# Optimization experiments

Measured on AMD Instinct MI355X. Metric: run time of the kernel, lower is better.

Reference implementation:

```python
import jax, jax.numpy as jnp
import numpy as np

B, C_IN, H, W = 4, 256, 48, 48
HEADS, HD = 8, 64
N = H * W
SCALE = 1.0 / (HD ** 0.5)


def setup_inputs() -> dict:
    key = jax.random.key(0)
    ks = jax.random.split(key, 5)
    x = jax.random.normal(ks[0], (B, C_IN, H, W), dtype=jnp.float32)
    # 1x1 conv weights, squeezed: [heads, head_channels, in_channels]
    Wq = jax.random.normal(ks[1], (HEADS, HD, C_IN), dtype=jnp.float32) * (C_IN ** -0.5)
    Wk = jax.random.normal(ks[2], (HEADS, HD, C_IN), dtype=jnp.float32) * (C_IN ** -0.5)
    Wv = jax.random.normal(ks[3], (HEADS, HD, C_IN), dtype=jnp.float32) * (C_IN ** -0.5)
    # output 1x1 conv: [in_channels, heads*head_channels]
    Wo = jax.random.normal(ks[4], (C_IN, HEADS * HD), dtype=jnp.float32) * ((HEADS * HD) ** -0.5)
    return {"x": x, "Wq": Wq, "Wk": Wk, "Wv": Wv, "Wo": Wo}


def reference(x, Wq, Wk, Wv, Wo):
    b, c, h, w = x.shape
    n = h * w
    xf = x.reshape(b, c, n)  # [B, C, N]
    # per-head 1x1 convs == batched projections -> [heads, B, N, HD]
    q = jnp.einsum('hdc,bcn->hbnd', Wq, xf)
    k = jnp.einsum('hdc,bcn->hbnd', Wk, xf)
    v = jnp.einsum('hdc,bcn->hbnd', Wv, xf)
    scores = jnp.einsum('hbnd,hbmd->hbnm', q, k) * SCALE  # [heads, B, N, N]
    probs = jax.nn.softmax(scores, axis=-1)
    ws = jnp.einsum('hbnm,hbmd->hbnd', probs, v)  # [heads, B, N, HD]
    # faithful replication of torch: transpose(1,2) then reshape(B, heads*HD, H, W)
    ws = jnp.transpose(ws, (0, 2, 1, 3))  # [heads, N, B, HD]
    ws = ws.reshape(b, HEADS * HD, h, w)
    out = jnp.einsum('oc,bchw->bohw', Wo, ws)  # output 1x1 conv
    return out
```

## Files before the change

### kernel.cpp

```cpp
#include <hip/hip_runtime.h>

#define B_     4
#define CIN    256
#define NTOK   2304
#define HEADS  8
#define HD     64
#define SCALE  0.125f
#define LOG2E  1.44269504088896f
#define QSCALE (SCALE * LOG2E)
#define PBIAS  4.0f
#define QKV_ELEMS (HEADS * B_ * NTOK * HD)
#define HBSTRIDE 147456
#define WSZ    131072

typedef _Float16 f16;
typedef _Float16 __attribute__((ext_vector_type(8))) h8v;
typedef _Float16 __attribute__((ext_vector_type(4))) h4v;
typedef ushort   __attribute__((ext_vector_type(8))) us8;
typedef float    __attribute__((ext_vector_type(16))) f16v;

__device__ inline uint pk2(float a, float b) {
    auto v = __builtin_amdgcn_cvt_pkrtz(a, b);
    return __builtin_bit_cast(uint, v);
}
#define EXP2(x) __builtin_amdgcn_exp2f(x)

#define GLOAD_LDS(g, l) __builtin_amdgcn_global_load_lds( \
    (const __attribute__((address_space(1))) unsigned int*)(g), \
    (__attribute__((address_space(3))) unsigned int*)(l), 16, 0, 0)

__global__ __launch_bounds__(256) void prep(
    const float* __restrict__ x,
    const float* __restrict__ Wq, const float* __restrict__ Wk,
    const float* __restrict__ Wv, const float* __restrict__ Wo,
    f16* __restrict__ wc, f16* __restrict__ woc, f16* __restrict__ xt)
{
    __shared__ float T[64][65];
    const int bid = blockIdx.x;
    const int tid = threadIdx.x;

    if (bid < 512) {
        int e4 = (bid * 256 + tid) * 4;
        const float* src; f16* dst; float mult = 1.0f; int off;
        if (e4 < WSZ)          { src = Wq; off = e4;           dst = wc;           mult = QSCALE; }
        else if (e4 < 2 * WSZ) { src = Wk; off = e4 - WSZ;     dst = wc + WSZ; }
        else if (e4 < 3 * WSZ) { src = Wv; off = e4 - 2 * WSZ; dst = wc + 2 * WSZ; }
        else                   { src = Wo; off = e4 - 3 * WSZ; dst = woc; }
        float4 r = *(const float4*)(src + off);
        h4v hv;
        hv.x = (f16)(r.x * mult); hv.y = (f16)(r.y * mult);
        hv.z = (f16)(r.z * mult); hv.w = (f16)(r.w * mult);
        *(h4v*)(dst + off) = hv;
        return;
    }

    const int r  = bid - 512;
    const int n0 = (r % 36) * 64;
    const int c0 = ((r / 36) % 4) * 64;
    const int b  = r / 144;
    const float* sb = x + ((size_t)b * CIN + c0) * NTOK;
    #pragma unroll
    for (int i = 0; i < 16; ++i) {
        int idx = tid + 256 * i;
        int rr = idx >> 6, ll = idx & 63;
        T[ll][rr] = sb[(size_t)rr * NTOK + n0 + ll];
    }
    __syncthreads();
    const size_t ob = ((size_t)b * NTOK + n0) * CIN + c0;
    #pragma unroll
    for (int i = 0; i < 4; ++i) {
        int idx = tid + 256 * i;
        int row = idx >> 4, c4 = (idx & 15) * 4;
        h4v v;
        v.x = (f16)T[row][c4 + 0]; v.y = (f16)T[row][c4 + 1];
        v.z = (f16)T[row][c4 + 2]; v.w = (f16)T[row][c4 + 3];
        *(h4v*)(xt + ob + (size_t)row * CIN + c4) = v;
    }
}

__global__ __launch_bounds__(128) void proj_mfma(
    const f16* __restrict__ wc, const f16* __restrict__ xt,
    f16* __restrict__ qh, f16* __restrict__ kh, f16* __restrict__ vth)
{
    const int ntile = blockIdx.x;
    const int hp    = blockIdx.y;
    const int b     = blockIdx.z;
    const int p     = hp >> 3, h = hp & 7;
    const int hb    = h * 4 + b;
    const f16* Wp = wc + ((size_t)p * 8 + h) * (HD * CIN);

    __shared__ __align__(16) f16 Ws[2][64][64], Xs[2][64][64];

    const int tid = threadIdx.x;
    const int w = tid >> 6, lane = tid & 63;
    const int lm = lane & 31, lh = lane >> 5;
    const int n_loc  = w * 32 + lm;
    const int n_glob = ntile * 64 + n_loc;

    const f16* xb = xt + ((size_t)b * NTOK + ntile * 64) * CIN;

    auto stage = [&](int buf, int c0) {
        const f16* src = (w == 0) ? Wp : xb;
        f16* dst = (w == 0) ? &Ws[buf][0][0] : &Xs[buf][0][0];
        #pragma unroll
        for (int i = 0; i < 8; ++i) {
            int g = i * 64 + lane; int row = g >> 3; int c = (g & 7) ^ (row & 7);
            GLOAD_LDS(src + (size_t)row * CIN + c0 + c * 8, dst + i * 512);
        }
    };

    f16v o0, o1;
    #pragma unroll
    for (int i = 0; i < 16; ++i) { o0[i] = 0.f; o1[i] = 0.f; }

    stage(0, 0);
    for (int c0 = 0; c0 < CIN; c0 += 64) {
        const int cur = (c0 >> 6) & 1;
        __syncthreads();
        if (c0 + 64 < CIN) stage(cur ^ 1, c0 + 64);
        #pragma unroll
        for (int s = 0; s < 4; ++s) {
            const int pp = ((2 * s + lh) ^ (lm & 7)) * 8;
            h8v a0 = *(const h8v*)&Ws[cur][lm][pp];
            h8v a1 = *(const h8v*)&Ws[cur][lm + 32][pp];
            h8v bh = *(const h8v*)&Xs[cur][n_loc][pp];
            o0 = __builtin_amdgcn_mfma_f32_32x32x16_f16(a0, bh, o0, 0, 0, 0);
            o1 = __builtin_amdgcn_mfma_f32_32x32x16_f16(a1, bh, o1, 0, 0, 0);
        }
    }

    const size_t hboff = (size_t)hb * HBSTRIDE;
    if (p < 2) {
        f16* oh = ((p == 0) ? qh : kh) + hboff + (size_t)n_glob * 64;
        #pragma unroll
        for (int t = 0; t < 2; ++t) {
            const f16v& oc = t ? o1 : o0;
            #pragma unroll
            for (int g = 0; g < 4; ++g) {
                int d0 = 8 * g + 4 * lh + 32 * t;
                h4v hv;
                hv.x = (f16)oc[4 * g + 0]; hv.y = (f16)oc[4 * g + 1];
                hv.z = (f16)oc[4 * g + 2]; hv.w = (f16)oc[4 * g + 3];
                *(h4v*)(oh + d0) = hv;
            }
        }
    } else {
        f16* oh = vth + hboff;
        #pragma unroll
        for (int t = 0; t < 2; ++t) {
            const f16v& oc = t ? o1 : o0;
            #pragma unroll
            for (int r = 0; r < 16; ++r) {
                int d = (r & 3) + 8 * (r >> 2) + 4 * lh + 32 * t;
                oh[(size_t)d * NTOK + n_glob] = (f16)oc[r];
            }
        }
    }
}

__global__ __launch_bounds__(128, 2) void attn_mfma(
    const f16* __restrict__ qh, const f16* __restrict__ kh,
    const f16* __restrict__ vth, f16* __restrict__ wsth)
{
    const int bid   = blockIdx.x;
    const int xcd   = bid & 7;
    const int slot  = bid >> 3;
    const int hb    = xcd * 4 + (slot / 18);
    const int rtile = slot % 18;
    const int h_    = hb >> 2, b = hb & 3;
    const int tid   = threadIdx.x;
    const int w     = tid >> 6;
    const int lane  = tid & 63;
    const int lm    = lane & 31;
    const int lh    = lane >> 5;

    __shared__ __align__(16) f16 SMEM[2][2][64][64];

    const size_t hboff = (size_t)hb * HBSTRIDE;
    const int mA = rtile * 128 + w * 64 + lm;
    const int mB = mA + 32;

    h8v QfA[4], QfB[4];
    #pragma unroll
    for (int s = 0; s < 4; ++s) {
        QfA[s] = *(const h8v*)(qh + hboff + (size_t)mA * 64 + (2 * s + lh) * 8);
        QfB[s] = *(const h8v*)(qh + hboff + (size_t)mB * 64 + (2 * s + lh) * 8);
    }

    f16v oA0, oA1, oB0, oB1;
    #pragma unroll
    for (int i = 0; i < 16; ++i) { oA0[i] = 0.f; oA1[i] = 0.f; oB0[i] = 0.f; oB1[i] = 0.f; }
    float lsumA = 0.f, lsumB = 0.f;

    const f16* gb = (w == 0) ? kh + hboff : vth + hboff;

    auto stage = [&](int buf, int kt) {
        f16* dst = &SMEM[buf][w][0][0];
        #pragma unroll
        for (int i = 0; i < 8; ++i) {
            int g   = i * 64 + lane;
            int row = g >> 3;
            int c   = (g & 7) ^ (row & 7);
            const f16* src = (w == 0)
                ? gb + kt * 4096 + row * 64 + c * 8
                : gb + (size_t)row * 2304 + kt * 64 + c * 8;
            GLOAD_LDS(src, dst + i * 512);
        }
    };

    stage(0, 0);
    __syncthreads();

    for (int kt = 0; kt < 36; ++kt) {
        const int cur = kt & 1;
        if (kt + 1 < 36) stage(cur ^ 1, kt + 1);

        f16v sA0, sA1, sB0, sB1;
        #pragma unroll
        for (int i = 0; i < 16; ++i) {
            sA0[i] = -PBIAS; sA1[i] = -PBIAS; sB0[i] = -PBIAS; sB1[i] = -PBIAS;
        }

        __builtin_amdgcn_s_setprio(1);
        #pragma unroll
        for (int s = 0; s < 4; ++s) {
            const int p = ((2 * s + lh) ^ (lm & 7)) * 8;
            h8v k0 = *(const h8v*)&SMEM[cur][0][lm][p];
            h8v k1 = *(const h8v*)&SMEM[cur][0][lm + 32][p];
            sA0 = __builtin_amdgcn_mfma_f32_32x32x16_f16(k0, QfA[s], sA0, 0, 0, 0);
            sA1 = __builtin_amdgcn_mfma_f32_32x32x16_f16(k1, QfA[s], sA1, 0, 0, 0);
            sB0 = __builtin_amdgcn_mfma_f32_32x32x16_f16(k0, QfB[s], sB0, 0, 0, 0);
            sB1 = __builtin_amdgcn_mfma_f32_32x32x16_f16(k1, QfB[s], sB1, 0, 0, 0);
        }
        __builtin_amdgcn_s_setprio(0);

        float rsA = 0.f, rsB = 0.f;
        #pragma unroll
        for (int i = 0; i < 16; ++i) { sA0[i] = EXP2(sA0[i]); rsA += sA0[i]; }
        #pragma unroll
        for (int i = 0; i < 16; ++i) { sA1[i] = EXP2(sA1[i]); rsA += sA1[i]; }
        #pragma unroll
        for (int i = 0; i < 16; ++i) { sB0[i] = EXP2(sB0[i]); rsB += sB0[i]; }
        #pragma unroll
        for (int i = 0; i < 16; ++i) { sB1[i] = EXP2(sB1[i]); rsB += sB1[i]; }
        lsumA += rsA; lsumB += rsB;

        uint PpkA[2][8], PpkB[2][8];
        #pragma unroll
        for (int pr = 0; pr < 8; ++pr) {
            PpkA[0][pr] = pk2(sA0[2 * pr], sA0[2 * pr + 1]);
            PpkA[1][pr] = pk2(sA1[2 * pr], sA1[2 * pr + 1]);
            PpkB[0][pr] = pk2(sB0[2 * pr], sB0[2 * pr + 1]);
            PpkB[1][pr] = pk2(sB1[2 * pr], sB1[2 * pr + 1]);
        }

        h8v pfA[4], pfB[4];
        #pragma unroll
        for (int s = 0; s < 4; ++s) {
            const int jt = s >> 1, q = 4 * (s & 1);
            auto a02 = __builtin_amdgcn_permlane32_swap(
                PpkA[jt][q + 0], PpkA[jt][q + 2], false, false);
            auto a13 = __builtin_amdgcn_permlane32_swap(
                PpkA[jt][q + 1], PpkA[jt][q + 3], false, false);
            uint4 ua = { a02[0], a13[0], a02[1], a13[1] };
            pfA[s] = __builtin_bit_cast(h8v, ua);
            auto b02 = __builtin_amdgcn_permlane32_swap(
                PpkB[jt][q + 0], PpkB[jt][q + 2], false, false);
            auto b13 = __builtin_amdgcn_permlane32_swap(
                PpkB[jt][q + 1], PpkB[jt][q + 3], false, false);
            uint4 ub = { b02[0], b13[0], b02[1], b13[1] };
            pfB[s] = __builtin_bit_cast(h8v, ub);
        }

        __builtin_amdgcn_s_setprio(1);
        #pragma unroll
        for (int s = 0; s < 4; ++s) {
            const int p = ((2 * s + lh) ^ (lm & 7)) * 8;
            h8v v0 = *(const h8v*)&SMEM[cur][1][lm][p];
            h8v v1 = *(const h8v*)&SMEM[cur][1][lm + 32][p];
            oA0 = __builtin_amdgcn_mfma_f32_32x32x16_f16(v0, pfA[s], oA0, 0, 0, 0);
            oA1 = __builtin_amdgcn_mfma_f32_32x32x16_f16(v1, pfA[s], oA1, 0, 0, 0);
            oB0 = __builtin_amdgcn_mfma_f32_32x32x16_f16(v0, pfB[s], oB0, 0, 0, 0);
            oB1 = __builtin_amdgcn_mfma_f32_32x32x16_f16(v1, pfB[s], oB1, 0, 0, 0);
        }
        __builtin_amdgcn_s_setprio(0);

        __syncthreads();
    }

    lsumA += __shfl_xor(lsumA, 32);
    lsumB += __shfl_xor(lsumB, 32);
    float invA = 1.0f / lsumA, invB = 1.0f / lsumB;

    f16* wrA = wsth + ((size_t)h_ * NTOK + mA) * 256 + b * 64;
    f16* wrB = wsth + ((size_t)h_ * NTOK + mB) * 256 + b * 64;
    #pragma unroll
    for (int g = 0; g < 4; ++g) {
        h4v r0, r1;
        r0.x = (f16)(oA0[4 * g + 0] * invA); r0.y = (f16)(oA0[4 * g + 1] * invA);
        r0.z = (f16)(oA0[4 * g + 2] * invA); r0.w = (f16)(oA0[4 * g + 3] * invA);
        *(h4v*)(wrA + 8 * g + 4 * lh) = r0;
        r1.x = (f16)(oA1[4 * g + 0] * invA); r1.y = (f16)(oA1[4 * g + 1] * invA);
        r1.z = (f16)(oA1[4 * g + 2] * invA); r1.w = (f16)(oA1[4 * g + 3] * invA);
        *(h4v*)(wrA + 32 + 8 * g + 4 * lh) = r1;
    }
    #pragma unroll
    for (int g = 0; g < 4; ++g) {
        h4v r0, r1;
        r0.x = (f16)(oB0[4 * g + 0] * invB); r0.y = (f16)(oB0[4 * g + 1] * invB);
        r0.z = (f16)(oB0[4 * g + 2] * invB); r0.w = (f16)(oB0[4 * g + 3] * invB);
        *(h4v*)(wrB + 8 * g + 4 * lh) = r0;
        r1.x = (f16)(oB1[4 * g + 0] * invB); r1.y = (f16)(oB1[4 * g + 1] * invB);
        r1.z = (f16)(oB1[4 * g + 2] * invB); r1.w = (f16)(oB1[4 * g + 3] * invB);
        *(h4v*)(wrB + 32 + 8 * g + 4 * lh) = r1;
    }
}

__global__ __launch_bounds__(128) void outconv_mfma(
    const f16* __restrict__ woc, const f16* __restrict__ ws,
    float* __restrict__ out)
{
    const int ntile = blockIdx.x;
    const int otile = blockIdx.y;
    const int b     = blockIdx.z;

    __shared__ __align__(16) f16 Wos[2][64][64];
    __shared__ __align__(16) f16 Xs[2][64][72];

    const int tid = threadIdx.x;
    const int w = tid >> 6, lane = tid & 63;
    const int lm = lane & 31, lh = lane >> 5;
    const int n_loc  = w * 32 + lm;
    const int n_glob = ntile * 64 + n_loc;
    const int pr = tid >> 2;
    const int qn = tid & 3;

    const f16* Wb = woc + (size_t)(otile * 64) * 512;
    const f16* wsb = ws + (size_t)b * 512 * NTOK + ntile * 64 + qn * 16;

    auto stageW = [&](int buf, int c0) {
        #pragma unroll
        for (int j = 0; j < 4; ++j) {
            int i = w * 4 + j;
            int g = i * 64 + lane; int row = g >> 3; int c = (g & 7) ^ (row & 7);
            GLOAD_LDS(Wb + (size_t)row * 512 + c0 + c * 8,
                      &Wos[buf][0][0] + i * 512);
        }
    };

    uint4 x0, x1, x2, x3;
    auto loadB = [&](int c0) {
        const f16* r0 = wsb + (size_t)(c0 + 2 * pr) * NTOK;
        const f16* r1 = r0 + NTOK;
        x0 = *(const uint4*)(r0);
        x1 = *(const uint4*)(r0 + 8);
        x2 = *(const uint4*)(r1);
        x3 = *(const uint4*)(r1 + 8);
    };
    auto storeB = [&](int buf) {
        us8 a0 = __builtin_bit_cast(us8, x0), a1 = __builtin_bit_cast(us8, x1);
        us8 b0 = __builtin_bit_cast(us8, x2), b1 = __builtin_bit_cast(us8, x3);
        #pragma unroll
        for (int j = 0; j < 8; ++j) {
            *(uint*)&Xs[buf][qn * 16 + j][2 * pr]     = (uint)a0[j] | ((uint)b0[j] << 16);
            *(uint*)&Xs[buf][qn * 16 + 8 + j][2 * pr] = (uint)a1[j] | ((uint)b1[j] << 16);
        }
    };

    f16v o0, o1;
    #pragma unroll
    for (int i = 0; i < 16; ++i) { o0[i] = 0.f; o1[i] = 0.f; }

    stageW(0, 0);
    loadB(0);
    storeB(0);
    for (int c0 = 0; c0 < 512; c0 += 64) {
        const int cur = (c0 >> 6) & 1;
        __syncthreads();
        if (c0 + 64 < 512) { stageW(cur ^ 1, c0 + 64); loadB(c0 + 64); }
        #pragma unroll
        for (int s = 0; s < 4; ++s) {
            const int pp = ((2 * s + lh) ^ (lm & 7)) * 8;
            const int co = (2 * s + lh) * 8;
            h8v a0 = *(const h8v*)&Wos[cur][lm][pp];
            h8v a1 = *(const h8v*)&Wos[cur][lm + 32][pp];
            h8v bh = *(const h8v*)&Xs[cur][n_loc][co];
            o0 = __builtin_amdgcn_mfma_f32_32x32x16_f16(a0, bh, o0, 0, 0, 0);
            o1 = __builtin_amdgcn_mfma_f32_32x32x16_f16(a1, bh, o1, 0, 0, 0);
        }
        if (c0 + 64 < 512) storeB(cur ^ 1);
    }

    #pragma unroll
    for (int t = 0; t < 2; ++t) {
        const f16v& oc = t ? o1 : o0;
        #pragma unroll
        for (int r = 0; r < 16; ++r) {
            int orow = otile * 64 + (r & 3) + 8 * (r >> 2) + 4 * lh + 32 * t;
            out[((size_t)b * CIN + orow) * NTOK + n_glob] = oc[r];
        }
    }
}

extern "C" void kernel_launch(void* const* d_in, const int* in_sizes, int n_in,
                              void* d_out, int out_size, void* d_ws, size_t ws_size,
                              hipStream_t stream)
{
    const float* x  = (const float*)d_in[0];
    const float* Wq = (const float*)d_in[1];
    const float* Wk = (const float*)d_in[2];
    const float* Wv = (const float*)d_in[3];
    const float* Wo = (const float*)d_in[4];
    float* out = (float*)d_out;

    f16* qh   = (f16*)d_ws;
    f16* kh   = qh   + QKV_ELEMS;
    f16* vth  = kh   + QKV_ELEMS;
    f16* wsth = vth  + QKV_ELEMS;
    f16* xt   = wsth;
    f16* wc   = wsth + QKV_ELEMS;
    f16* woc  = wc   + 3 * WSZ;

    prep<<<dim3(1088), 256, 0, stream>>>(x, Wq, Wk, Wv, Wo, wc, woc, xt);
    proj_mfma<<<dim3(36, 24, 4), 128, 0, stream>>>(wc, xt, qh, kh, vth);
    attn_mfma<<<dim3(576), 128, 0, stream>>>(qh, kh, vth, wsth);
    outconv_mfma<<<dim3(36, 4, 4), 128, 0, stream>>>(woc, wsth, out);
}
```

Before: 178.9 us.

## Split attention key loop across wave pairs with LDS reduction of partial outputs

```diff
diff --git a/kernel.cpp b/kernel.cpp
--- a/kernel.cpp
+++ b/kernel.cpp
@@ -158,7 +158,7 @@
     }
 }
 
-__global__ __launch_bounds__(128, 2) void attn_mfma(
+__global__ __launch_bounds__(256, 2) void attn_mfma(
     const f16* __restrict__ qh, const f16* __restrict__ kh,
     const f16* __restrict__ vth, f16* __restrict__ wsth)
 {
@@ -166,18 +166,21 @@
     const int xcd   = bid & 7;
     const int slot  = bid >> 3;
     const int hb    = xcd * 4 + (slot / 18);
-    const int rtile = slot % 18;
+    const int rpair = slot % 18;
     const int h_    = hb >> 2, b = hb & 3;
     const int tid   = threadIdx.x;
     const int w     = tid >> 6;
     const int lane  = tid & 63;
     const int lm    = lane & 31;
     const int lh    = lane >> 5;
+    const int qg    = w >> 1;
+    const int ks    = w & 1;
 
     __shared__ __align__(16) f16 SMEM[2][2][64][64];
+    __shared__ float LRED[256];
 
     const size_t hboff = (size_t)hb * HBSTRIDE;
-    const int mA = rtile * 128 + w * 64 + lm;
+    const int mA = rpair * 128 + qg * 64 + lm;
     const int mB = mA + 32;
 
     h8v QfA[4], QfB[4];
@@ -192,29 +195,29 @@
     for (int i = 0; i < 16; ++i) { oA0[i] = 0.f; oA1[i] = 0.f; oB0[i] = 0.f; oB1[i] = 0.f; }
     float lsumA = 0.f, lsumB = 0.f;
 
-    const f16* gb = (w == 0) ? kh + hboff : vth + hboff;
-
-    auto stage = [&](int buf, int kt) {
-        f16* dst = &SMEM[buf][w][0][0];
+    const int  sv  = w >> 1;
+    const int  stp = w & 1;
+    const f16* gb  = (sv == 0) ? kh + hboff : vth + hboff;
+
+    auto stage = [&](int st) {
+        const int kts = 2 * st + stp;
+        f16* dst = &SMEM[sv][stp][0][0];
         #pragma unroll
         for (int i = 0; i < 8; ++i) {
             int g   = i * 64 + lane;
             int row = g >> 3;
             int c   = (g & 7) ^ (row & 7);
-            const f16* src = (w == 0)
-                ? gb + kt * 4096 + row * 64 + c * 8
-                : gb + (size_t)row * 2304 + kt * 64 + c * 8;
+            const f16* src = (sv == 0)
+                ? gb + kts * 4096 + row * 64 + c * 8
+                : gb + (size_t)row * 2304 + kts * 64 + c * 8;
             GLOAD_LDS(src, dst + i * 512);
         }
     };
 
-    stage(0, 0);
+    stage(0);
     __syncthreads();
 
-    for (int kt = 0; kt < 36; ++kt) {
-        const int cur = kt & 1;
-        if (kt + 1 < 36) stage(cur ^ 1, kt + 1);
-
+    for (int st = 0; st < 18; ++st) {
         f16v sA0, sA1, sB0, sB1;
         #pragma unroll
         for (int i = 0; i < 16; ++i) {
@@ -225,8 +228,8 @@
         #pragma unroll
         for (int s = 0; s < 4; ++s) {
             const int p = ((2 * s + lh) ^ (lm & 7)) * 8;
-            h8v k0 = *(const h8v*)&SMEM[cur][0][lm][p];
-            h8v k1 = *(const h8v*)&SMEM[cur][0][lm + 32][p];
+            h8v k0 = *(const h8v*)&SMEM[0][ks][lm][p];
+            h8v k1 = *(const h8v*)&SMEM[0][ks][lm + 32][p];
             sA0 = __builtin_amdgcn_mfma_f32_32x32x16_f16(k0, QfA[s], sA0, 0, 0, 0);
             sA1 = __builtin_amdgcn_mfma_f32_32x32x16_f16(k1, QfA[s], sA1, 0, 0, 0);
             sB0 = __builtin_amdgcn_mfma_f32_32x32x16_f16(k0, QfB[s], sB0, 0, 0, 0);
@@ -234,16 +237,41 @@
         }
         __builtin_amdgcn_s_setprio(0);
 
-        float rsA = 0.f, rsB = 0.f;
-        #pragma unroll
-        for (int i = 0; i < 16; ++i) { sA0[i] = EXP2(sA0[i]); rsA += sA0[i]; }
-        #pragma unroll
-        for (int i = 0; i < 16; ++i) { sA1[i] = EXP2(sA1[i]); rsA += sA1[i]; }
-        #pragma unroll
-        for (int i = 0; i < 16; ++i) { sB0[i] = EXP2(sB0[i]); rsB += sB0[i]; }
-        #pragma unroll
-        for (int i = 0; i < 16; ++i) { sB1[i] = EXP2(sB1[i]); rsB += sB1[i]; }
-        lsumA += rsA; lsumB += rsB;
+        __syncthreads();
+        if (st + 1 < 18 && sv == 0) stage(st + 1);
+
+        float pa0 = 0.f, pa1 = 0.f, pa2 = 0.f, pa3 = 0.f;
+        float pb0 = 0.f, pb1 = 0.f, pb2 = 0.f, pb3 = 0.f;
+        #pragma unroll
+        for (int i = 0; i < 16; i += 4) {
+            sA0[i+0] = EXP2(sA0[i+0]); pa0 += sA0[i+0];
+            sA0[i+1] = EXP2(sA0[i+1]); pa1 += sA0[i+1];
+            sA0[i+2] = EXP2(sA0[i+2]); pa2 += sA0[i+2];
+            sA0[i+3] = EXP2(sA0[i+3]); pa3 += sA0[i+3];
+        }
+        #pragma unroll
+        for (int i = 0; i < 16; i += 4) {
+            sA1[i+0] = EXP2(sA1[i+0]); pa0 += sA1[i+0];
+            sA1[i+1] = EXP2(sA1[i+1]); pa1 += sA1[i+1];
+            sA1[i+2] = EXP2(sA1[i+2]); pa2 += sA1[i+2];
+            sA1[i+3] = EXP2(sA1[i+3]); pa3 += sA1[i+3];
+        }
+        #pragma unroll
+        for (int i = 0; i < 16; i += 4) {
+            sB0[i+0] = EXP2(sB0[i+0]); pb0 += sB0[i+0];
+            sB0[i+1] = EXP2(sB0[i+1]); pb1 += sB0[i+1];
+            sB0[i+2] = EXP2(sB0[i+2]); pb2 += sB0[i+2];
+            sB0[i+3] = EXP2(sB0[i+3]); pb3 += sB0[i+3];
+        }
+        #pragma unroll
+        for (int i = 0; i < 16; i += 4) {
+            sB1[i+0] = EXP2(sB1[i+0]); pb0 += sB1[i+0];
+            sB1[i+1] = EXP2(sB1[i+1]); pb1 += sB1[i+1];
+            sB1[i+2] = EXP2(sB1[i+2]); pb2 += sB1[i+2];
+            sB1[i+3] = EXP2(sB1[i+3]); pb3 += sB1[i+3];
+        }
+        lsumA += (pa0 + pa1) + (pa2 + pa3);
+        lsumB += (pb0 + pb1) + (pb2 + pb3);
 
         uint PpkA[2][8], PpkB[2][8];
         #pragma unroll
@@ -276,8 +304,8 @@
         #pragma unroll
         for (int s = 0; s < 4; ++s) {
             const int p = ((2 * s + lh) ^ (lm & 7)) * 8;
-            h8v v0 = *(const h8v*)&SMEM[cur][1][lm][p];
-            h8v v1 = *(const h8v*)&SMEM[cur][1][lm + 32][p];
+            h8v v0 = *(const h8v*)&SMEM[1][ks][lm][p];
+            h8v v1 = *(const h8v*)&SMEM[1][ks][lm + 32][p];
             oA0 = __builtin_amdgcn_mfma_f32_32x32x16_f16(v0, pfA[s], oA0, 0, 0, 0);
             oA1 = __builtin_amdgcn_mfma_f32_32x32x16_f16(v1, pfA[s], oA1, 0, 0, 0);
             oB0 = __builtin_amdgcn_mfma_f32_32x32x16_f16(v0, pfB[s], oB0, 0, 0, 0);
@@ -286,33 +314,58 @@
         __builtin_amdgcn_s_setprio(0);
 
         __syncthreads();
-    }
-
-    lsumA += __shfl_xor(lsumA, 32);
-    lsumB += __shfl_xor(lsumB, 32);
-    float invA = 1.0f / lsumA, invB = 1.0f / lsumB;
-
-    f16* wrA = wsth + ((size_t)h_ * NTOK + mA) * 256 + b * 64;
-    f16* wrB = wsth + ((size_t)h_ * NTOK + mB) * 256 + b * 64;
-    #pragma unroll
-    for (int g = 0; g < 4; ++g) {
-        h4v r0, r1;
-        r0.x = (f16)(oA0[4 * g + 0] * invA); r0.y = (f16)(oA0[4 * g + 1] * invA);
-        r0.z = (f16)(oA0[4 * g + 2] * invA); r0.w = (f16)(oA0[4 * g + 3] * invA);
-        *(h4v*)(wrA + 8 * g + 4 * lh) = r0;
-        r1.x = (f16)(oA1[4 * g + 0] * invA); r1.y = (f16)(oA1[4 * g + 1] * invA);
-        r1.z = (f16)(oA1[4 * g + 2] * invA); r1.w = (f16)(oA1[4 * g + 3] * invA);
-        *(h4v*)(wrA + 32 + 8 * g + 4 * lh) = r1;
-    }
-    #pragma unroll
-    for (int g = 0; g < 4; ++g) {
-        h4v r0, r1;
-        r0.x = (f16)(oB0[4 * g + 0] * invB); r0.y = (f16)(oB0[4 * g + 1] * invB);
-        r0.z = (f16)(oB0[4 * g + 2] * invB); r0.w = (f16)(oB0[4 * g + 3] * invB);
-        *(h4v*)(wrB + 8 * g + 4 * lh) = r0;
-        r1.x = (f16)(oB1[4 * g + 0] * invB); r1.y = (f16)(oB1[4 * g + 1] * invB);
-        r1.z = (f16)(oB1[4 * g + 2] * invB); r1.w = (f16)(oB1[4 * g + 3] * invB);
-        *(h4v*)(wrB + 32 + 8 * g + 4 * lh) = r1;
+        if (st + 1 < 18 && sv == 1) stage(st + 1);
+    }
+
+    float* red = (float*)&SMEM[0][0][0][0];
+    if (ks == 1) {
+        float* dA = red + (size_t)(qg * 128 + lane) * 32;
+        float* dB = red + (size_t)(qg * 128 + 64 + lane) * 32;
+        #pragma unroll
+        for (int i = 0; i < 16; ++i) {
+            dA[i] = oA0[i]; dA[16 + i] = oA1[i];
+            dB[i] = oB0[i]; dB[16 + i] = oB1[i];
+        }
+        LRED[qg * 128 + lane] = lsumA;
+        LRED[qg * 128 + 64 + lane] = lsumB;
+    }
+    __syncthreads();
+    if (ks == 0) {
+        const float* sA = red + (size_t)(qg * 128 + lane) * 32;
+        const float* sB = red + (size_t)(qg * 128 + 64 + lane) * 32;
+        #pragma unroll
+        for (int i = 0; i < 16; ++i) {
+            oA0[i] += sA[i]; oA1[i] += sA[16 + i];
+            oB0[i] += sB[i]; oB1[i] += sB[16 + i];
+        }
+        lsumA += LRED[qg * 128 + lane];
+        lsumB += LRED[qg * 128 + 64 + lane];
+        lsumA += __shfl_xor(lsumA, 32);
+        lsumB += __shfl_xor(lsumB, 32);
+        float invA = 1.0f / lsumA, invB = 1.0f / lsumB;
+
+        f16* wrA = wsth + ((size_t)h_ * NTOK + mA) * 256 + b * 64;
+        f16* wrB = wsth + ((size_t)h_ * NTOK + mB) * 256 + b * 64;
+        #pragma unroll
+        for (int g = 0; g < 4; ++g) {
+            h4v r0, r1;
+            r0.x = (f16)(oA0[4 * g + 0] * invA); r0.y = (f16)(oA0[4 * g + 1] * invA);
+            r0.z = (f16)(oA0[4 * g + 2] * invA); r0.w = (f16)(oA0[4 * g + 3] * invA);
+            *(h4v*)(wrA + 8 * g + 4 * lh) = r0;
+            r1.x = (f16)(oA1[4 * g + 0] * invA); r1.y = (f16)(oA1[4 * g + 1] * invA);
+            r1.z = (f16)(oA1[4 * g + 2] * invA); r1.w = (f16)(oA1[4 * g + 3] * invA);
+            *(h4v*)(wrA + 32 + 8 * g + 4 * lh) = r1;
+        }
+        #pragma unroll
+        for (int g = 0; g < 4; ++g) {
+            h4v r0, r1;
+            r0.x = (f16)(oB0[4 * g + 0] * invB); r0.y = (f16)(oB0[4 * g + 1] * invB);
+            r0.z = (f16)(oB0[4 * g + 2] * invB); r0.w = (f16)(oB0[4 * g + 3] * invB);
+            *(h4v*)(wrB + 8 * g + 4 * lh) = r0;
+            r1.x = (f16)(oB1[4 * g + 0] * invB); r1.y = (f16)(oB1[4 * g + 1] * invB);
+            r1.z = (f16)(oB1[4 * g + 2] * invB); r1.w = (f16)(oB1[4 * g + 3] * invB);
+            *(h4v*)(wrB + 32 + 8 * g + 4 * lh) = r1;
+        }
     }
 }
 
@@ -423,6 +476,6 @@
 
     prep<<<dim3(1088), 256, 0, stream>>>(x, Wq, Wk, Wv, Wo, wc, woc, xt);
     proj_mfma<<<dim3(36, 24, 4), 128, 0, stream>>>(wc, xt, qh, kh, vth);
-    attn_mfma<<<dim3(576), 128, 0, stream>>>(qh, kh, vth, wsth);
+    attn_mfma<<<dim3(576), 256, 0, stream>>>(qh, kh, vth, wsth);
     outconv_mfma<<<dim3(36, 4, 4), 128, 0, stream>>>(woc, wsth, out);
 }
```

Result: faster. 169.2 us (-5.4%).
